# Performance work log

Measured on AMD Instinct MI355X. Metric: run time of the kernel, lower is better.

Reference implementation:

```python
import jax, jax.numpy as jnp
import numpy as np

B, H, Q_TOK, D = 8, 12, 577, 64
N_SIDE = 24  # 24x24 = 576 patches, +1 CLS row/col -> 577


def _pairwise_dists():
    rows, cols = np.indices((N_SIDE, N_SIDE))
    idx = np.stack([rows.flatten(), cols.flatten()], axis=-1).astype(np.float32)  # (576, 2)
    d = idx[:, None, :] - idx[None, :, :]  # (576, 576, 2)
    d = np.pad(d, ((1, 0), (1, 0), (0, 0)))  # zero-pad CLS token row/col -> (577, 577, 2)
    return jnp.asarray(d)


def setup_inputs() -> dict:
    key = jax.random.key(0)
    ks = jax.random.split(key, 4)
    query = jax.random.normal(ks[0], (B, H, Q_TOK, D), jnp.float32)
    W1 = jax.random.normal(ks[1], (D, 64), jnp.float32) * 0.05
    b1 = jnp.zeros((64,), jnp.float32)
    W2 = jax.random.normal(ks[2], (64, 3), jnp.float32) * 0.05
    b2 = jnp.zeros((3,), jnp.float32)
    # uniform noise for RelaxedBernoulli reparameterized sample
    u = jax.random.uniform(ks[3], (B, H, Q_TOK, Q_TOK), jnp.float32, 1e-6, 1.0 - 1e-6)
    temperature = jnp.ones((1,), jnp.float32)
    return {"query": query, "W1": W1, "b1": b1, "W2": W2, "b2": b2,
            "dists": _pairwise_dists(), "u": u, "temperature": temperature}


def reference(query, W1, b1, W2, b2, dists, u, temperature):
    # sigma MLP: Linear -> exact GELU -> Linear, per (b,h,q) token
    hdn = jax.nn.gelu(query @ W1 + b1, approximate=False)
    sig = hdn @ W2 + b2  # (b,h,q,3)
    sy = jnp.exp(sig[..., 0]) + 1.0
    sx = jnp.exp(sig[..., 1]) + 1.0
    rho = jnp.tanh(sig[..., 2]) * 0.99
    cov = sy * sx * rho
    # 2x2 covariance matrix per query: [[sy^2, sy*sx*rho],[sy*sx*rho, sx^2]]
    Sigma = jnp.stack([jnp.stack([sy * sy, cov], -1),
                       jnp.stack([cov, sx * sx], -1)], -2)  # (b,h,q,2,2)
    # closed-form 2x2 inverse (same math as torch.linalg.inv)
    det = (sy * sx) ** 2 * (1.0 - rho * rho)
    inv00 = (sx * sx) / det
    inv11 = (sy * sy) / det
    inv01 = -cov / det
    dy = dists[..., 0]  # (q,k)
    dx = dists[..., 1]
    # Mahalanobis quadratic form, fused (no (b,h,q,k,2,2) intermediates)
    quad = (inv00[..., None] * (dy * dy)
            + 2.0 * inv01[..., None] * (dy * dx)
            + inv11[..., None] * (dx * dx))  # (b,h,q,k)
    kernel = jnp.exp(-0.5 * quad)
    probs = kernel / jnp.max(kernel, axis=-1, keepdims=True)
    probs = jnp.minimum(probs, 1.0)
    # RelaxedBernoulli rsample: sigmoid((logit(p) + logistic_noise) / T)
    logits = jnp.log(probs) - jnp.log1p(-probs)
    noise = jnp.log(u) - jnp.log1p(-u)
    mask = jax.nn.sigmoid((logits + noise) / temperature[0])
    return mask, Sigma
```

## Files before the change

### kernel.cpp

```cpp
#include <hip/hip_runtime.h>
#include <math.h>

constexpr int BB = 8, HH = 12, QT = 577, DD = 64;
constexpr int NTOK = BB * HH * QT;
constexpr long long MASK_ELEMS = (long long)NTOK * QT;
constexpr long long NVEC = MASK_ELEMS / 4;
constexpr int MASK_BLOCKS = (int)((NVEC + 255) / 256);

using f4 = __attribute__((ext_vector_type(4))) float;

__global__ __launch_bounds__(256)
void mlp_sigma(const float* __restrict__ query,
               const float* __restrict__ W1,
               const float* __restrict__ b1,
               const float* __restrict__ W2,
               const float* __restrict__ b2,
               f4* __restrict__ Sig)
{
    const int token = (blockIdx.x * 256 + threadIdx.x) >> 6;
    const int lane  = threadIdx.x & 63;
    if (token >= NTOK) return;

    const float qv = query[(size_t)token * DD + lane];
    float acc = b1[lane];
#pragma unroll
    for (int i = 0; i < DD; ++i)
        acc = fmaf(__shfl(qv, i), W1[i * DD + lane], acc);
    const float h = 0.5f * acc * (1.0f + erff(acc * 0.7071067811865476f));

    float p0 = h * W2[lane * 3 + 0];
    float p1 = h * W2[lane * 3 + 1];
    float p2 = h * W2[lane * 3 + 2];
#pragma unroll
    for (int off = 32; off > 0; off >>= 1) {
        p0 += __shfl_xor(p0, off);
        p1 += __shfl_xor(p1, off);
        p2 += __shfl_xor(p2, off);
    }
    if (lane == 0) {
        const float sy  = expf(p0 + b2[0]) + 1.0f;
        const float sx  = expf(p1 + b2[1]) + 1.0f;
        const float rho = tanhf(p2 + b2[2]) * 0.99f;
        const float cov = sy * sx * rho;
        f4 s; s.x = sy * sy; s.y = cov; s.z = cov; s.w = sx * sx;
        Sig[token] = s;
    }
}

__global__ __launch_bounds__(256)
void mask_flat(const float* __restrict__ u,
               const float* __restrict__ temp,
               float* __restrict__ out)
{
    const f4* __restrict__ Sig = (const f4*)(out + MASK_ELEMS);
    const long long v = (long long)blockIdx.x * 256 + threadIdx.x;
    if (v >= NVEC) return;
    const unsigned e0 = (unsigned)(v * 4);

    const float invT = 1.0f / temp[0];
    const f4 uv4 = *(const f4*)(u + e0);
    f4 m4;

#pragma unroll
    for (int c = 0; c < 4; ++c) {
        const unsigned e     = e0 + (unsigned)c;
        const unsigned token = e / 577u;
        const unsigned k     = e - token * 577u;
        const unsigned q     = token - (token / 577u) * 577u;

        const int qm1 = (q > 0u) ? (int)q - 1 : 0;
        const int km1 = (k > 0u) ? (int)k - 1 : 0;
        const int qr = qm1 / 24, qcc = qm1 - qr * 24;
        const int kr = km1 / 24, kcc = km1 - kr * 24;
        float dy = (float)(qr - kr);
        float dx = (float)(qcc - kcc);
        if ((q == 0u) | (k == 0u)) { dy = 0.0f; dx = 0.0f; }

        const f4 S = Sig[token];
        const float det2 = 2.0f * fmaf(S.x, S.w, -S.y * S.y);
        const float qraw = fmaf(S.w, dy * dy,
                           fmaf(-2.0f * S.y, dy * dx, S.x * (dx * dx)));
        const float hq = fmaxf(qraw * __fdividef(1.0f, det2), 0.0f);
        const float E  = __expf(hq);
        const float a  = E - 1.0f;
        const float uv = uv4[c];
        float m = __fdividef(uv, fmaf(a, 1.0f - uv, uv));
        if (invT != 1.0f) {
            const float rr = __fdividef(a * (1.0f - uv), uv);
            m = __fdividef(1.0f, 1.0f + __expf(__logf(rr) * invT));
        }
        m4[c] = m;
    }
    __builtin_nontemporal_store(m4, (f4*)(out + e0));
}

extern "C" void kernel_launch(void* const* d_in, const int* in_sizes, int n_in,
                              void* d_out, int out_size, void* d_ws, size_t ws_size,
                              hipStream_t stream) {
    const float* query = (const float*)d_in[0];
    const float* W1    = (const float*)d_in[1];
    const float* b1    = (const float*)d_in[2];
    const float* W2    = (const float*)d_in[3];
    const float* b2    = (const float*)d_in[4];
    const float* u     = (const float*)d_in[6];
    const float* temp  = (const float*)d_in[7];
    float* out = (float*)d_out;

    f4* Sig = (f4*)(out + MASK_ELEMS);
    mlp_sigma<<<dim3(NTOK / 4), dim3(256), 0, stream>>>(query, W1, b1, W2, b2, Sig);
    mask_flat<<<dim3(MASK_BLOCKS), dim3(256), 0, stream>>>(u, temp, out);
}
```

Baseline: 298.5 us.

## Restructure mask kernel by query row with shared-memory distance table

The flat per-element mask kernel is replaced by one where each block handles a single query index across 32 batch-head rows. The distance products (dy², dy·dx, dx²) for that query are computed once into shared memory, and the inverse-covariance coefficients are computed once per row. This removes the per-element integer divisions by 577 and 24 and the repeated Sigma loads. The cost is more complex alignment and tail handling, plus less parallelism per block, since each wave loops over 8 rows serially.

New measurement: 313.2 us. 4.9% more time.

```diff
diff --git a/kernel.cpp b/kernel.cpp
--- a/kernel.cpp
+++ b/kernel.cpp
@@ -4,8 +4,10 @@
 constexpr int BB = 8, HH = 12, QT = 577, DD = 64;
 constexpr int NTOK = BB * HH * QT;
 constexpr long long MASK_ELEMS = (long long)NTOK * QT;
-constexpr long long NVEC = MASK_ELEMS / 4;
-constexpr int MASK_BLOCKS = (int)((NVEC + 255) / 256);
+constexpr int NBH = BB * HH;
+constexpr int ROWS_PER_WAVE = 8;
+constexpr int ROWS_PER_BLOCK = 4 * ROWS_PER_WAVE;
+constexpr int CHUNKS = NBH / ROWS_PER_BLOCK;
 
 using f4 = __attribute__((ext_vector_type(4))) float;
 
@@ -48,50 +50,103 @@
 }
 
 __global__ __launch_bounds__(256)
-void mask_flat(const float* __restrict__ u,
-               const float* __restrict__ temp,
-               float* __restrict__ out)
+void mask_rows_v(const float* __restrict__ u,
+                 const float* __restrict__ temp,
+                 float* __restrict__ out)
 {
+    __shared__ f4 G4[640];
+
     const f4* __restrict__ Sig = (const f4*)(out + MASK_ELEMS);
-    const long long v = (long long)blockIdx.x * 256 + threadIdx.x;
-    if (v >= NVEC) return;
-    const unsigned e0 = (unsigned)(v * 4);
+    const int q     = blockIdx.x;
+    const int chunk = blockIdx.y;
+    const int wave  = threadIdx.x >> 6;
+    const int lane  = threadIdx.x & 63;
+
+    {
+        const int qm1 = (q > 0) ? q - 1 : 0;
+        const int qr  = (int)((unsigned)qm1 / 24u);
+        const int qc  = qm1 - qr * 24;
+        const float fqr = (float)qr, fqc = (float)qc;
+        const bool qz = (q == 0);
+        for (int k = threadIdx.x; k < QT; k += 256) {
+            const int km1 = (k > 0) ? k - 1 : 0;
+            const int kr  = (int)((unsigned)km1 / 24u);
+            const int kc  = km1 - kr * 24;
+            float dy = fqr - (float)kr;
+            float dx = fqc - (float)kc;
+            if (qz | (k == 0)) { dy = 0.0f; dx = 0.0f; }
+            f4 g; g.x = dy * dy; g.y = dy * dx; g.z = dx * dx; g.w = 0.0f;
+            G4[(k & 3) * 160 + (k >> 2)] = g;
+        }
+    }
+    __syncthreads();
 
     const float invT = 1.0f / temp[0];
-    const f4 uv4 = *(const f4*)(u + e0);
-    f4 m4;
+    const int bh0 = chunk * ROWS_PER_BLOCK + wave * ROWS_PER_WAVE;
+
+#pragma unroll 1
+    for (int r = 0; r < ROWS_PER_WAVE; ++r) {
+        const int token = (bh0 + r) * QT + q;
+        const f4 S = Sig[token];
+        const float rdet = __fdividef(1.0f, fmaf(S.x, S.w, -S.y * S.y));
+        const float j0 =  0.5f * S.w * rdet;
+        const float j1 = -S.y * rdet;
+        const float j2 =  0.5f * S.x * rdet;
+
+        const unsigned base = (unsigned)token * (unsigned)QT;
+        const int h  = (int)((0u - base) & 3u);
+        const int NV = (QT - h) >> 2;
+
+        const float* __restrict__ up = u   + base + h;
+        float*       __restrict__ mp = out + base + h;
+
+        int bc[4];
+#pragma unroll
+        for (int c = 0; c < 4; ++c)
+            bc[c] = ((h + c) & 3) * 160 + ((h + c) >> 2);
 
 #pragma unroll
-    for (int c = 0; c < 4; ++c) {
-        const unsigned e     = e0 + (unsigned)c;
-        const unsigned token = e / 577u;
-        const unsigned k     = e - token * 577u;
-        const unsigned q     = token - (token / 577u) * 577u;
+        for (int p = 0; p < 3; ++p) {
+            const int idx = p * 64 + lane;
+            if (idx < NV) {
+                const f4 uu = *(const f4*)(up + 4 * idx);
+                f4 m4;
+#pragma unroll
+                for (int c = 0; c < 4; ++c) {
+                    const f4 g = G4[bc[c] + idx];
+                    const float hq = fmaxf(
+                        fmaf(j2, g.z, fmaf(j1, g.y, j0 * g.x)), 0.0f);
+                    const float E  = __expf(hq);
+                    const float a  = E - 1.0f;
+                    const float uv = uu[c];
+                    float m = __fdividef(uv, fmaf(a, 1.0f - uv, uv));
+                    if (invT != 1.0f) {
+                        const float rr = __fdividef(a * (1.0f - uv), uv);
+                        m = __fdividef(1.0f, 1.0f + __expf(__logf(rr) * invT));
+                    }
+                    m4[c] = m;
+                }
+                __builtin_nontemporal_store(m4, (f4*)(mp + 4 * idx));
+            }
+        }
 
-        const int qm1 = (q > 0u) ? (int)q - 1 : 0;
-        const int km1 = (k > 0u) ? (int)k - 1 : 0;
-        const int qr = qm1 / 24, qcc = qm1 - qr * 24;
-        const int kr = km1 / 24, kcc = km1 - kr * 24;
-        float dy = (float)(qr - kr);
-        float dx = (float)(qcc - kcc);
-        if ((q == 0u) | (k == 0u)) { dy = 0.0f; dx = 0.0f; }
-
-        const f4 S = Sig[token];
-        const float det2 = 2.0f * fmaf(S.x, S.w, -S.y * S.y);
-        const float qraw = fmaf(S.w, dy * dy,
-                           fmaf(-2.0f * S.y, dy * dx, S.x * (dx * dx)));
-        const float hq = fmaxf(qraw * __fdividef(1.0f, det2), 0.0f);
-        const float E  = __expf(hq);
-        const float a  = E - 1.0f;
-        const float uv = uv4[c];
-        float m = __fdividef(uv, fmaf(a, 1.0f - uv, uv));
-        if (invT != 1.0f) {
-            const float rr = __fdividef(a * (1.0f - uv), uv);
-            m = __fdividef(1.0f, 1.0f + __expf(__logf(rr) * invT));
+        const int scnt = QT - 4 * NV;
+        if (lane < scnt) {
+            const int k = (lane < h) ? lane : (h + 4 * NV + (lane - h));
+            const f4 g = G4[(k & 3) * 160 + (k >> 2)];
+            const float hq = fmaxf(
+                fmaf(j2, g.z, fmaf(j1, g.y, j0 * g.x)), 0.0f);
+            const float E  = __expf(hq);
+            const float a  = E - 1.0f;
+            const float uv = u[base + k];
+            float m = __fdividef(uv, fmaf(a, 1.0f - uv, uv));
+            if (invT != 1.0f) {
+                const float rr = __fdividef(a * (1.0f - uv), uv);
+                m = __fdividef(1.0f, 1.0f + __expf(__logf(rr) * invT));
+            }
+            __builtin_nontemporal_store(m, out + base + k);
         }
-        m4[c] = m;
     }
-    __builtin_nontemporal_store(m4, (f4*)(out + e0));
 }
 
 extern "C" void kernel_launch(void* const* d_in, const int* in_sizes, int n_in,
@@ -108,5 +163,5 @@
 
     f4* Sig = (f4*)(out + MASK_ELEMS);
     mlp_sigma<<<dim3(NTOK / 4), dim3(256), 0, stream>>>(query, W1, b1, W2, b2, Sig);
-    mask_flat<<<dim3(MASK_BLOCKS), dim3(256), 0, stream>>>(u, temp, out);
+    mask_rows_v<<<dim3(QT, CHUNKS), dim3(256), 0, stream>>>(u, temp, out);
 }
```
